# Optimization experiments

Measured on AMD Instinct MI355X. Metric: run time of the kernel, lower is better.

## Reference

```python
import jax, jax.numpy as jnp
import numpy as np

N = 100000        # nodes
E = 3200000       # edges (avg degree 32)
F_IN = 512        # input node features
HIDDEN = 16       # hardcoded in GCN.__init__
NUM_CLASSES = 40


def setup_inputs() -> dict:
    key = jax.random.key(0)
    k1, k2, k3, k4 = jax.random.split(key, 4)
    edge_index = jax.random.randint(k1, (2, E), 0, N, dtype=jnp.int32)
    x = jax.random.normal(k2, (N, F_IN), dtype=jnp.float32)
    # GCNConv weights (glorot-ish scale) and biases
    W1 = jax.random.normal(k3, (F_IN, HIDDEN), dtype=jnp.float32) * (1.0 / np.sqrt(F_IN))
    b1 = jnp.zeros((HIDDEN,), dtype=jnp.float32)
    W2 = jax.random.normal(k4, (HIDDEN, NUM_CLASSES), dtype=jnp.float32) * (1.0 / np.sqrt(HIDDEN))
    b2 = jnp.zeros((NUM_CLASSES,), dtype=jnp.float32)
    return {"edge_index": edge_index, "x": x, "W1": W1, "b1": b1, "W2": W2, "b2": b2}


def _gcn_conv(x, src, dst, W, b, n):
    # PyG GCNConv: linear transform, symmetric-normalized scatter-add aggregation
    h = x @ W                                             # [N, out]
    deg = jax.ops.segment_sum(jnp.ones_like(dst, dtype=h.dtype), dst, num_segments=n)
    dinv = jnp.where(deg > 0, jax.lax.rsqrt(deg), 0.0)    # deg^{-1/2}
    norm = dinv[src] * dinv[dst]                          # [E_total]
    out = jax.ops.segment_sum(h[src] * norm[:, None], dst, num_segments=n)
    return out + b


def reference(edge_index, x, W1, b1, W2, b2):
    n = x.shape[0]
    # GCNConv adds self-loops by default
    loop = jnp.arange(n, dtype=edge_index.dtype)
    src = jnp.concatenate([edge_index[0], loop])
    dst = jnp.concatenate([edge_index[1], loop])
    h = _gcn_conv(x, src, dst, W1, b1, n)
    h = jax.nn.relu(h)
    # F.dropout(training=self.training) -> identity in eval mode
    h = _gcn_conv(h, src, dst, W2, b2, n)
    return jax.nn.log_softmax(h, axis=1)[::20]
```

## Files before the change

### kernel.cpp

```cpp
#include <hip/hip_runtime.h>
#include <hip/hip_bf16.h>
#include <cstdint>
#include <math.h>

#define F_IN 512
#define HID  16
#define NCLS 40
#define OUT_STRIDE 20
#define TB   256
#define NBA  256
#define CAP  16384

typedef __attribute__((ext_vector_type(8))) short short8;
typedef __attribute__((ext_vector_type(4))) float f32x4;

__device__ inline unsigned short f2bf(float f) {
    unsigned u = __float_as_uint(f);
    u += 0x7fff + ((u >> 16) & 1);
    return (unsigned short)(u >> 16);
}
__device__ inline float bf2f(unsigned v) {
    return __uint_as_float(v << 16);
}

__global__ __launch_bounds__(256) void k_mega1(const float* __restrict__ x,
                                               const float* __restrict__ W1,
                                               unsigned short* __restrict__ h1b,
                                               const int* __restrict__ src,
                                               const int* __restrict__ dst,
                                               int* __restrict__ gcnt,
                                               unsigned* __restrict__ bin,
                                               int E, int NB, int chunk,
                                               int n, int GB) {
    __shared__ uint4 bl[16 * 64];
    int t = threadIdx.x;

    if ((int)blockIdx.x < GB) {
        for (int f = t; f < 16 * 64; f += 256) {
            int kstep = f >> 6, ln = f & 63;
            int col = ln & 15, k0 = kstep * 32 + (ln >> 4) * 8;
            unsigned up[4];
#pragma unroll
            for (int i = 0; i < 4; i++) {
                float a = W1[(k0 + 2 * i) * HID + col];
                float b = W1[(k0 + 2 * i + 1) * HID + col];
                up[i] = (unsigned)f2bf(a) | ((unsigned)f2bf(b) << 16);
            }
            bl[f] = make_uint4(up[0], up[1], up[2], up[3]);
        }
        __syncthreads();

        int wid = t >> 6, lane = t & 63;
        int rows0 = blockIdx.x * 256 + wid * 64;
        int arow = lane & 15, kgrp = lane >> 4;

        const float* xr[4];
#pragma unroll
        for (int rt = 0; rt < 4; rt++) {
            int r = rows0 + rt * 16 + arow;
            if (r >= n) r = n - 1;
            xr[rt] = x + (size_t)r * F_IN + kgrp * 8;
        }

        f32x4 acc[4];
#pragma unroll
        for (int rt = 0; rt < 4; rt++) acc[rt] = (f32x4){0.f, 0.f, 0.f, 0.f};

#pragma unroll 4
        for (int kstep = 0; kstep < 16; kstep++) {
            uint4 braw = bl[kstep * 64 + lane];
            short8 b;
            *(uint4*)&b = braw;
#pragma unroll
            for (int rt = 0; rt < 4; rt++) {
                f32x4 lo = __builtin_nontemporal_load((const f32x4*)(xr[rt] + kstep * 32));
                f32x4 hi = __builtin_nontemporal_load((const f32x4*)(xr[rt] + kstep * 32 + 4));
                __hip_bfloat162 c0 = __float22bfloat162_rn(make_float2(lo[0], lo[1]));
                __hip_bfloat162 c1 = __float22bfloat162_rn(make_float2(lo[2], lo[3]));
                __hip_bfloat162 c2 = __float22bfloat162_rn(make_float2(hi[0], hi[1]));
                __hip_bfloat162 c3 = __float22bfloat162_rn(make_float2(hi[2], hi[3]));
                uint4 araw;
                __builtin_memcpy(&araw.x, &c0, 4);
                __builtin_memcpy(&araw.y, &c1, 4);
                __builtin_memcpy(&araw.z, &c2, 4);
                __builtin_memcpy(&araw.w, &c3, 4);
                short8 a;
                *(uint4*)&a = araw;
                acc[rt] = __builtin_amdgcn_mfma_f32_16x16x32_bf16(a, b, acc[rt], 0, 0, 0);
            }
        }

        int col = lane & 15, rbase = (lane >> 4) * 4;
#pragma unroll
        for (int rt = 0; rt < 4; rt++) {
#pragma unroll
            for (int r = 0; r < 4; r++) {
                int row = rows0 + rt * 16 + rbase + r;
                if (row < n)
                    h1b[(size_t)row * HID + col] = f2bf(acc[rt][r]);
            }
        }
        return;
    }

    int blk = blockIdx.x - GB;
    int* h = (int*)bl;
    int* pos = h + 512;
    for (int b = t; b < NB; b += 256) h[b] = 0;
    __syncthreads();
    int e0 = blk * chunk, e1 = min(E, e0 + chunk);
    int nvec = (e1 - e0) >> 2;
    const int4* d4 = (const int4*)(dst + e0);
    const int4* s4 = (const int4*)(src + e0);
    for (int i = t; i < nvec; i += 256) {
        int4 d = d4[i];
        atomicAdd(&h[d.x >> 8], 1);
        atomicAdd(&h[d.y >> 8], 1);
        atomicAdd(&h[d.z >> 8], 1);
        atomicAdd(&h[d.w >> 8], 1);
    }
    for (int e = e0 + nvec * 4 + t; e < e1; e += 256)
        atomicAdd(&h[dst[e] >> 8], 1);
    __syncthreads();
    for (int b = t; b < NB; b += 256) {
        int c = h[b];
        int rb = c ? atomicAdd(&gcnt[b], c) : 0;
        pos[b] = b * CAP + rb;
    }
    __syncthreads();
    for (int i = t; i < nvec; i += 256) {
        int4 d = d4[i];
        int4 s = s4[i];
        int p;
        p = atomicAdd(&pos[d.x >> 8], 1); bin[p] = ((unsigned)s.x << 8) | (unsigned)(d.x & (TB - 1));
        p = atomicAdd(&pos[d.y >> 8], 1); bin[p] = ((unsigned)s.y << 8) | (unsigned)(d.y & (TB - 1));
        p = atomicAdd(&pos[d.z >> 8], 1); bin[p] = ((unsigned)s.z << 8) | (unsigned)(d.z & (TB - 1));
        p = atomicAdd(&pos[d.w >> 8], 1); bin[p] = ((unsigned)s.w << 8) | (unsigned)(d.w & (TB - 1));
    }
    for (int e = e0 + nvec * 4 + t; e < e1; e += 256) {
        int d = dst[e], s = src[e];
        int p = atomicAdd(&pos[d >> 8], 1);
        bin[p] = ((unsigned)s << 8) | (unsigned)(d & (TB - 1));
    }
}

__global__ __launch_bounds__(256) void k_sortb2(const unsigned* __restrict__ bin,
                                                const int* __restrict__ gcnt,
                                                int* __restrict__ csr,
                                                int2* __restrict__ rng,
                                                float* __restrict__ dinv,
                                                unsigned short* __restrict__ h1b,
                                                int N) {
    __shared__ int cnt[TB], incl[TB], pos[TB];
    int t = threadIdx.x, b = blockIdx.x;
    cnt[t] = 0;
    __syncthreads();
    int j0 = b * CAP, count = gcnt[b];
    for (int j = t; j < count; j += 256)
        atomicAdd(&cnt[bin[j0 + j] & (TB - 1)], 1);
    __syncthreads();
    incl[t] = cnt[t];
    __syncthreads();
    for (int off = 1; off < TB; off <<= 1) {
        int v = (t >= off) ? incl[t - off] : 0;
        __syncthreads();
        incl[t] += v;
        __syncthreads();
    }
    int ex = incl[t] - cnt[t];
    pos[t] = ex;
    int node = b * TB + t;
    float dv = rsqrtf((float)cnt[t] + 1.0f);
    if (node < N) {
        rng[node] = make_int2(j0 + ex, j0 + ex + cnt[t]);
        dinv[node] = dv;
        uint4* p = (uint4*)(h1b + (size_t)node * HID);
        uint4 lo = p[0], hi = p[1];
        unsigned w[8] = {lo.x, lo.y, lo.z, lo.w, hi.x, hi.y, hi.z, hi.w};
#pragma unroll
        for (int i = 0; i < 8; i++) {
            float a = bf2f(w[i] & 0xffff) * dv;
            float c = bf2f(w[i] >> 16) * dv;
            w[i] = (unsigned)f2bf(a) | ((unsigned)f2bf(c) << 16);
        }
        p[0] = make_uint4(w[0], w[1], w[2], w[3]);
        p[1] = make_uint4(w[4], w[5], w[6], w[7]);
    }
    __syncthreads();
    for (int j = t; j < count; j += 256) {
        unsigned v = bin[j0 + j];
        int pp = atomicAdd(&pos[v & (TB - 1)], 1);
        csr[j0 + pp] = (int)(v >> 8);
    }
}

__global__ __launch_bounds__(256) void k_agg(const uint2* __restrict__ h1u2,
                                             const int* __restrict__ csr,
                                             const int2* __restrict__ rng,
                                             const float* __restrict__ dinv,
                                             const float* __restrict__ b1,
                                             uint2* __restrict__ zu2, int n) {
    int lane = threadIdx.x & 63;
    int wave0 = (blockIdx.x * blockDim.x + threadIdx.x) >> 6;
    int nwaves = (gridDim.x * blockDim.x) >> 6;
    int c2 = lane & 3;
    int sub = lane >> 2;
    float bl0 = b1[4 * c2 + 0], bl1 = b1[4 * c2 + 1];
    float bl2 = b1[4 * c2 + 2], bl3 = b1[4 * c2 + 3];
    for (int node = wave0; node < n; node += nwaves) {
        int2 r = rng[node];
        int s0 = r.x, s1 = r.y;
        uint2 us = h1u2[(size_t)node * 4 + c2];
        float s[4] = {0.f, 0.f, 0.f, 0.f};
        int j = s0 + sub;
        int nxt = (j < s1) ? __builtin_nontemporal_load(&csr[j]) : 0;
        for (; j < s1; j += 16) {
            int cur = nxt;
            int jn = j + 16;
            if (jn < s1) nxt = __builtin_nontemporal_load(&csr[jn]);
            uint2 u = h1u2[(size_t)cur * 4 + c2];
            s[0] += bf2f(u.x & 0xffff); s[1] += bf2f(u.x >> 16);
            s[2] += bf2f(u.y & 0xffff); s[3] += bf2f(u.y >> 16);
        }
#pragma unroll
        for (int m = 4; m < 64; m <<= 1) {
            s[0] += __shfl_xor(s[0], m); s[1] += __shfl_xor(s[1], m);
            s[2] += __shfl_xor(s[2], m); s[3] += __shfl_xor(s[3], m);
        }
        s[0] += bf2f(us.x & 0xffff); s[1] += bf2f(us.x >> 16);
        s[2] += bf2f(us.y & 0xffff); s[3] += bf2f(us.y >> 16);
        float dv = dinv[node];
        float p0 = dv * s[0] + bl0;
        float p1 = dv * s[1] + bl1;
        float p2 = dv * s[2] + bl2;
        float p3 = dv * s[3] + bl3;
        if (lane < 4) {
            uint2 o;
            o.x = (unsigned)f2bf(fmaxf(p0, 0.f) * dv) | ((unsigned)f2bf(fmaxf(p1, 0.f) * dv) << 16);
            o.y = (unsigned)f2bf(fmaxf(p2, 0.f) * dv) | ((unsigned)f2bf(fmaxf(p3, 0.f) * dv) << 16);
            zu2[(size_t)node * 4 + c2] = o;
        }
    }
}

__global__ void k_out(const unsigned short* __restrict__ zb,
                      const int* __restrict__ csr, const int2* __restrict__ rng,
                      const float* __restrict__ dinv, const float* __restrict__ W2,
                      const float* __restrict__ b2, float* __restrict__ out, int nOut) {
    int lane = threadIdx.x & 63;
    int wv = (blockIdx.x * blockDim.x + threadIdx.x) >> 6;
    if (wv >= nOut) return;
    int node = wv * OUT_STRIDE;
    int c = lane & 15, sub = lane >> 4;
    int2 r = rng[node];
    int s0 = r.x, s1 = r.y;
    float sum = 0.f;
    for (int j = s0 + sub; j < s1; j += 4)
        sum += bf2f(zb[(size_t)__builtin_nontemporal_load(&csr[j]) * HID + c]);
    sum += __shfl_xor(sum, 16);
    sum += __shfl_xor(sum, 32);
    sum += bf2f(zb[(size_t)node * HID + c]);
    float a = dinv[node] * sum;

    int jj = lane < NCLS ? lane : 0;
    float v = 0.f;
#pragma unroll
    for (int cc = 0; cc < 16; cc++) {
        float ac = __shfl(a, cc);
        v = fmaf(ac, W2[cc * NCLS + jj], v);
    }
    v += b2[jj];

    float vm = lane < NCLS ? v : -INFINITY;
    for (int off = 1; off < 64; off <<= 1) vm = fmaxf(vm, __shfl_xor(vm, off));
    float ex = lane < NCLS ? expf(v - vm) : 0.f;
    float se = ex;
    for (int off = 1; off < 64; off <<= 1) se += __shfl_xor(se, off);
    float ls = logf(se);
    if (lane < NCLS) out[(size_t)wv * NCLS + lane] = v - vm - ls;
}

extern "C" void kernel_launch(void* const* d_in, const int* in_sizes, int n_in,
                              void* d_out, int out_size, void* d_ws, size_t ws_size,
                              hipStream_t stream) {
    const int E = in_sizes[0] / 2;
    const int N = in_sizes[1] / F_IN;
    const int nOut = (N + OUT_STRIDE - 1) / OUT_STRIDE;
    const int NB = (N + TB - 1) / TB;
    const int chunk = ((E + NBA - 1) / NBA + 3) & ~3;
    const int GB = (N + 255) / 256;

    const int* src = (const int*)d_in[0];
    const int* dst = src + E;
    const float* x  = (const float*)d_in[1];
    const float* W1 = (const float*)d_in[2];
    const float* b1 = (const float*)d_in[3];
    const float* W2 = (const float*)d_in[4];
    const float* b2 = (const float*)d_in[5];
    float* out = (float*)d_out;

    uint8_t* w = (uint8_t*)d_ws;
    size_t off = 0;
    auto carve = [&](size_t bytes) {
        void* p = w + off;
        off += (bytes + 15) & ~(size_t)15;
        return p;
    };
    float*          dinv  = (float*)carve((size_t)N * 4);
    int*            gcnt  = (int*)carve((size_t)NB * 4);
    unsigned*       bin   = (unsigned*)carve((size_t)NB * CAP * 4);
    int*            csr   = (int*)carve((size_t)NB * CAP * 4);
    int2*           rng   = (int2*)carve((size_t)N * 8);
    unsigned short* h1b   = (unsigned short*)carve((size_t)N * HID * 2);
    unsigned short* zb    = (unsigned short*)carve((size_t)N * HID * 2);
    (void)ws_size; (void)n_in; (void)out_size;

    (void)hipMemsetAsync(gcnt, 0, (size_t)NB * 4, stream);
    k_mega1<<<GB + NBA, 256, 0, stream>>>(x, W1, h1b, src, dst, gcnt, bin,
                                          E, NB, chunk, N, GB);
    k_sortb2<<<NB, TB, 0, stream>>>(bin, gcnt, csr, rng, dinv, h1b, N);
    k_agg  <<<2048, 256, 0, stream>>>((const uint2*)h1b, csr, rng, dinv, b1, (uint2*)zb, N);
    k_out  <<<(nOut * 64 + 255) / 256, 256, 0, stream>>>(zb, csr, rng, dinv, W2, b2, out, nOut);
}
```

Measured before the change: 171.9 us.

## Fuse all GCN stages into one cooperative persistent kernel with grid syncs

Replaces the four separate kernels with one cooperative kernel. Stage boundaries become grid.sync barriers, and the first 256 blocks do edge binning before joining a dynamic, atomic-counter tile queue for the x@W1 MFMA GEMM. This removes launch gaps between kernels and lets the binning and GEMM work balance across a persistent grid. In exchange, the grid is capped at 512-1024 blocks, so the later stages run with grid-stride loops instead of their original launch shapes, and each grid sync has its own cost.

```diff
diff --git a/kernel.cpp b/kernel.cpp
--- a/kernel.cpp
+++ b/kernel.cpp
@@ -1,14 +1,17 @@
 #include <hip/hip_runtime.h>
+#include <hip/hip_cooperative_groups.h>
 #include <hip/hip_bf16.h>
 #include <cstdint>
 #include <math.h>
+
+namespace cg = cooperative_groups;
 
 #define F_IN 512
 #define HID  16
 #define NCLS 40
 #define OUT_STRIDE 20
 #define TB   256
-#define NBA  256
+#define PARTB 256
 #define CAP  16384
 
 typedef __attribute__((ext_vector_type(8))) short short8;
@@ -23,261 +26,261 @@
     return __uint_as_float(v << 16);
 }
 
-__global__ __launch_bounds__(256) void k_mega1(const float* __restrict__ x,
-                                               const float* __restrict__ W1,
-                                               unsigned short* __restrict__ h1b,
-                                               const int* __restrict__ src,
-                                               const int* __restrict__ dst,
-                                               int* __restrict__ gcnt,
-                                               unsigned* __restrict__ bin,
-                                               int E, int NB, int chunk,
-                                               int n, int GB) {
+__global__ __launch_bounds__(256) void k_fused(
+    const float* __restrict__ x, const float* __restrict__ W1,
+    unsigned short* __restrict__ h1b,
+    const int* __restrict__ src, const int* __restrict__ dst,
+    int* __restrict__ gcnt, unsigned* __restrict__ bin,
+    int* __restrict__ csr, int2* __restrict__ rng, float* __restrict__ dinv,
+    unsigned short* __restrict__ zb, const float* __restrict__ b1,
+    const float* __restrict__ W2, const float* __restrict__ b2,
+    float* __restrict__ out,
+    int E, int N, int NB, int chunk, int GT, int* tilec, int nOut)
+{
+    cg::grid_group grid = cg::this_grid();
     __shared__ uint4 bl[16 * 64];
-    int t = threadIdx.x;
-
-    if ((int)blockIdx.x < GB) {
-        for (int f = t; f < 16 * 64; f += 256) {
-            int kstep = f >> 6, ln = f & 63;
-            int col = ln & 15, k0 = kstep * 32 + (ln >> 4) * 8;
-            unsigned up[4];
-#pragma unroll
-            for (int i = 0; i < 4; i++) {
-                float a = W1[(k0 + 2 * i) * HID + col];
-                float b = W1[(k0 + 2 * i + 1) * HID + col];
-                up[i] = (unsigned)f2bf(a) | ((unsigned)f2bf(b) << 16);
-            }
-            bl[f] = make_uint4(up[0], up[1], up[2], up[3]);
-        }
-        __syncthreads();
-
-        int wid = t >> 6, lane = t & 63;
-        int rows0 = blockIdx.x * 256 + wid * 64;
+    int t = threadIdx.x, blk = blockIdx.x;
+    int lane = t & 63;
+
+    if (blk < PARTB) {
+        int* h   = (int*)bl;
+        int* pos = h + 512;
+        for (int b = t; b < NB; b += 256) h[b] = 0;
+        __syncthreads();
+        int e0 = blk * chunk, e1 = min(E, e0 + chunk);
+        int nvec = (e1 - e0) >> 2;
+        const int4* d4 = (const int4*)(dst + e0);
+        const int4* s4 = (const int4*)(src + e0);
+        for (int i = t; i < nvec; i += 256) {
+            int4 d = d4[i];
+            atomicAdd(&h[d.x >> 8], 1);
+            atomicAdd(&h[d.y >> 8], 1);
+            atomicAdd(&h[d.z >> 8], 1);
+            atomicAdd(&h[d.w >> 8], 1);
+        }
+        for (int e = e0 + nvec * 4 + t; e < e1; e += 256)
+            atomicAdd(&h[dst[e] >> 8], 1);
+        __syncthreads();
+        for (int b = t; b < NB; b += 256) {
+            int c = h[b];
+            int rb = c ? atomicAdd(&gcnt[b], c) : 0;
+            pos[b] = b * CAP + rb;
+        }
+        __syncthreads();
+        for (int i = t; i < nvec; i += 256) {
+            int4 d = d4[i];
+            int4 s = s4[i];
+            int p;
+            p = atomicAdd(&pos[d.x >> 8], 1); bin[p] = ((unsigned)s.x << 8) | (unsigned)(d.x & (TB - 1));
+            p = atomicAdd(&pos[d.y >> 8], 1); bin[p] = ((unsigned)s.y << 8) | (unsigned)(d.y & (TB - 1));
+            p = atomicAdd(&pos[d.z >> 8], 1); bin[p] = ((unsigned)s.z << 8) | (unsigned)(d.z & (TB - 1));
+            p = atomicAdd(&pos[d.w >> 8], 1); bin[p] = ((unsigned)s.w << 8) | (unsigned)(d.w & (TB - 1));
+        }
+        for (int e = e0 + nvec * 4 + t; e < e1; e += 256) {
+            int d = dst[e], s = src[e];
+            int p = atomicAdd(&pos[d >> 8], 1);
+            bin[p] = ((unsigned)s << 8) | (unsigned)(d & (TB - 1));
+        }
+        __syncthreads();
+    }
+
+    for (int f = t; f < 16 * 64; f += 256) {
+        int kstep = f >> 6, ln = f & 63;
+        int col = ln & 15, k0 = kstep * 32 + (ln >> 4) * 8;
+        unsigned up[4];
+#pragma unroll
+        for (int i = 0; i < 4; i++) {
+            float a = W1[(k0 + 2 * i) * HID + col];
+            float b = W1[(k0 + 2 * i + 1) * HID + col];
+            up[i] = (unsigned)f2bf(a) | ((unsigned)f2bf(b) << 16);
+        }
+        bl[f] = make_uint4(up[0], up[1], up[2], up[3]);
+    }
+    __syncthreads();
+
+    {
         int arow = lane & 15, kgrp = lane >> 4;
-
-        const float* xr[4];
-#pragma unroll
-        for (int rt = 0; rt < 4; rt++) {
-            int r = rows0 + rt * 16 + arow;
-            if (r >= n) r = n - 1;
-            xr[rt] = x + (size_t)r * F_IN + kgrp * 8;
-        }
-
-        f32x4 acc[4];
-#pragma unroll
-        for (int rt = 0; rt < 4; rt++) acc[rt] = (f32x4){0.f, 0.f, 0.f, 0.f};
+        for (;;) {
+            int tl;
+            if (lane == 0) tl = atomicAdd(tilec, 1);
+            tl = __shfl(tl, 0);
+            if (tl >= GT) break;
+            int rows0 = tl * 64;
+
+            const float* xr[4];
+#pragma unroll
+            for (int rt = 0; rt < 4; rt++) {
+                int r = rows0 + rt * 16 + arow;
+                if (r >= N) r = N - 1;
+                xr[rt] = x + (size_t)r * F_IN + kgrp * 8;
+            }
+            f32x4 acc[4];
+#pragma unroll
+            for (int rt = 0; rt < 4; rt++) acc[rt] = (f32x4){0.f, 0.f, 0.f, 0.f};
 
 #pragma unroll 4
-        for (int kstep = 0; kstep < 16; kstep++) {
-            uint4 braw = bl[kstep * 64 + lane];
-            short8 b;
-            *(uint4*)&b = braw;
+            for (int kstep = 0; kstep < 16; kstep++) {
+                uint4 braw = bl[kstep * 64 + lane];
+                short8 b;
+                *(uint4*)&b = braw;
+#pragma unroll
+                for (int rt = 0; rt < 4; rt++) {
+                    f32x4 lo = __builtin_nontemporal_load((const f32x4*)(xr[rt] + kstep * 32));
+                    f32x4 hi = __builtin_nontemporal_load((const f32x4*)(xr[rt] + kstep * 32 + 4));
+                    __hip_bfloat162 c0 = __float22bfloat162_rn(make_float2(lo[0], lo[1]));
+                    __hip_bfloat162 c1 = __float22bfloat162_rn(make_float2(lo[2], lo[3]));
+                    __hip_bfloat162 c2 = __float22bfloat162_rn(make_float2(hi[0], hi[1]));
+                    __hip_bfloat162 c3 = __float22bfloat162_rn(make_float2(hi[2], hi[3]));
+                    uint4 araw;
+                    __builtin_memcpy(&araw.x, &c0, 4);
+                    __builtin_memcpy(&araw.y, &c1, 4);
+                    __builtin_memcpy(&araw.z, &c2, 4);
+                    __builtin_memcpy(&araw.w, &c3, 4);
+                    short8 a;
+                    *(uint4*)&a = araw;
+                    acc[rt] = __builtin_amdgcn_mfma_f32_16x16x32_bf16(a, b, acc[rt], 0, 0, 0);
+                }
+            }
+            int col = lane & 15, rbase = (lane >> 4) * 4;
 #pragma unroll
             for (int rt = 0; rt < 4; rt++) {
-                f32x4 lo = __builtin_nontemporal_load((const f32x4*)(xr[rt] + kstep * 32));
-                f32x4 hi = __builtin_nontemporal_load((const f32x4*)(xr[rt] + kstep * 32 + 4));
-                __hip_bfloat162 c0 = __float22bfloat162_rn(make_float2(lo[0], lo[1]));
-                __hip_bfloat162 c1 = __float22bfloat162_rn(make_float2(lo[2], lo[3]));
-                __hip_bfloat162 c2 = __float22bfloat162_rn(make_float2(hi[0], hi[1]));
-                __hip_bfloat162 c3 = __float22bfloat162_rn(make_float2(hi[2], hi[3]));
-                uint4 araw;
-                __builtin_memcpy(&araw.x, &c0, 4);
-                __builtin_memcpy(&araw.y, &c1, 4);
-                __builtin_memcpy(&araw.z, &c2, 4);
-                __builtin_memcpy(&araw.w, &c3, 4);
-                short8 a;
-                *(uint4*)&a = araw;
-                acc[rt] = __builtin_amdgcn_mfma_f32_16x16x32_bf16(a, b, acc[rt], 0, 0, 0);
-            }
-        }
-
-        int col = lane & 15, rbase = (lane >> 4) * 4;
-#pragma unroll
-        for (int rt = 0; rt < 4; rt++) {
-#pragma unroll
-            for (int r = 0; r < 4; r++) {
-                int row = rows0 + rt * 16 + rbase + r;
-                if (row < n)
-                    h1b[(size_t)row * HID + col] = f2bf(acc[rt][r]);
-            }
-        }
-        return;
-    }
-
-    int blk = blockIdx.x - GB;
-    int* h = (int*)bl;
-    int* pos = h + 512;
-    for (int b = t; b < NB; b += 256) h[b] = 0;
-    __syncthreads();
-    int e0 = blk * chunk, e1 = min(E, e0 + chunk);
-    int nvec = (e1 - e0) >> 2;
-    const int4* d4 = (const int4*)(dst + e0);
-    const int4* s4 = (const int4*)(src + e0);
-    for (int i = t; i < nvec; i += 256) {
-        int4 d = d4[i];
-        atomicAdd(&h[d.x >> 8], 1);
-        atomicAdd(&h[d.y >> 8], 1);
-        atomicAdd(&h[d.z >> 8], 1);
-        atomicAdd(&h[d.w >> 8], 1);
-    }
-    for (int e = e0 + nvec * 4 + t; e < e1; e += 256)
-        atomicAdd(&h[dst[e] >> 8], 1);
-    __syncthreads();
-    for (int b = t; b < NB; b += 256) {
-        int c = h[b];
-        int rb = c ? atomicAdd(&gcnt[b], c) : 0;
-        pos[b] = b * CAP + rb;
-    }
-    __syncthreads();
-    for (int i = t; i < nvec; i += 256) {
-        int4 d = d4[i];
-        int4 s = s4[i];
-        int p;
-        p = atomicAdd(&pos[d.x >> 8], 1); bin[p] = ((unsigned)s.x << 8) | (unsigned)(d.x & (TB - 1));
-        p = atomicAdd(&pos[d.y >> 8], 1); bin[p] = ((unsigned)s.y << 8) | (unsigned)(d.y & (TB - 1));
-        p = atomicAdd(&pos[d.z >> 8], 1); bin[p] = ((unsigned)s.z << 8) | (unsigned)(d.z & (TB - 1));
-        p = atomicAdd(&pos[d.w >> 8], 1); bin[p] = ((unsigned)s.w << 8) | (unsigned)(d.w & (TB - 1));
-    }
-    for (int e = e0 + nvec * 4 + t; e < e1; e += 256) {
-        int d = dst[e], s = src[e];
-        int p = atomicAdd(&pos[d >> 8], 1);
-        bin[p] = ((unsigned)s << 8) | (unsigned)(d & (TB - 1));
-    }
-}
-
-__global__ __launch_bounds__(256) void k_sortb2(const unsigned* __restrict__ bin,
-                                                const int* __restrict__ gcnt,
-                                                int* __restrict__ csr,
-                                                int2* __restrict__ rng,
-                                                float* __restrict__ dinv,
-                                                unsigned short* __restrict__ h1b,
-                                                int N) {
-    __shared__ int cnt[TB], incl[TB], pos[TB];
-    int t = threadIdx.x, b = blockIdx.x;
-    cnt[t] = 0;
-    __syncthreads();
-    int j0 = b * CAP, count = gcnt[b];
-    for (int j = t; j < count; j += 256)
-        atomicAdd(&cnt[bin[j0 + j] & (TB - 1)], 1);
-    __syncthreads();
-    incl[t] = cnt[t];
-    __syncthreads();
-    for (int off = 1; off < TB; off <<= 1) {
-        int v = (t >= off) ? incl[t - off] : 0;
-        __syncthreads();
-        incl[t] += v;
-        __syncthreads();
-    }
-    int ex = incl[t] - cnt[t];
-    pos[t] = ex;
-    int node = b * TB + t;
-    float dv = rsqrtf((float)cnt[t] + 1.0f);
-    if (node < N) {
-        rng[node] = make_int2(j0 + ex, j0 + ex + cnt[t]);
-        dinv[node] = dv;
-        uint4* p = (uint4*)(h1b + (size_t)node * HID);
-        uint4 lo = p[0], hi = p[1];
-        unsigned w[8] = {lo.x, lo.y, lo.z, lo.w, hi.x, hi.y, hi.z, hi.w};
-#pragma unroll
-        for (int i = 0; i < 8; i++) {
-            float a = bf2f(w[i] & 0xffff) * dv;
-            float c = bf2f(w[i] >> 16) * dv;
-            w[i] = (unsigned)f2bf(a) | ((unsigned)f2bf(c) << 16);
-        }
-        p[0] = make_uint4(w[0], w[1], w[2], w[3]);
-        p[1] = make_uint4(w[4], w[5], w[6], w[7]);
-    }
-    __syncthreads();
-    for (int j = t; j < count; j += 256) {
-        unsigned v = bin[j0 + j];
-        int pp = atomicAdd(&pos[v & (TB - 1)], 1);
-        csr[j0 + pp] = (int)(v >> 8);
-    }
-}
-
-__global__ __launch_bounds__(256) void k_agg(const uint2* __restrict__ h1u2,
-                                             const int* __restrict__ csr,
-                                             const int2* __restrict__ rng,
-                                             const float* __restrict__ dinv,
-                                             const float* __restrict__ b1,
-                                             uint2* __restrict__ zu2, int n) {
-    int lane = threadIdx.x & 63;
-    int wave0 = (blockIdx.x * blockDim.x + threadIdx.x) >> 6;
-    int nwaves = (gridDim.x * blockDim.x) >> 6;
-    int c2 = lane & 3;
-    int sub = lane >> 2;
-    float bl0 = b1[4 * c2 + 0], bl1 = b1[4 * c2 + 1];
-    float bl2 = b1[4 * c2 + 2], bl3 = b1[4 * c2 + 3];
-    for (int node = wave0; node < n; node += nwaves) {
-        int2 r = rng[node];
-        int s0 = r.x, s1 = r.y;
-        uint2 us = h1u2[(size_t)node * 4 + c2];
-        float s[4] = {0.f, 0.f, 0.f, 0.f};
-        int j = s0 + sub;
-        int nxt = (j < s1) ? __builtin_nontemporal_load(&csr[j]) : 0;
-        for (; j < s1; j += 16) {
-            int cur = nxt;
-            int jn = j + 16;
-            if (jn < s1) nxt = __builtin_nontemporal_load(&csr[jn]);
-            uint2 u = h1u2[(size_t)cur * 4 + c2];
-            s[0] += bf2f(u.x & 0xffff); s[1] += bf2f(u.x >> 16);
-            s[2] += bf2f(u.y & 0xffff); s[3] += bf2f(u.y >> 16);
-        }
-#pragma unroll
-        for (int m = 4; m < 64; m <<= 1) {
-            s[0] += __shfl_xor(s[0], m); s[1] += __shfl_xor(s[1], m);
-            s[2] += __shfl_xor(s[2], m); s[3] += __shfl_xor(s[3], m);
-        }
-        s[0] += bf2f(us.x & 0xffff); s[1] += bf2f(us.x >> 16);
-        s[2] += bf2f(us.y & 0xffff); s[3] += bf2f(us.y >> 16);
-        float dv = dinv[node];
-        float p0 = dv * s[0] + bl0;
-        float p1 = dv * s[1] + bl1;
-        float p2 = dv * s[2] + bl2;
-        float p3 = dv * s[3] + bl3;
-        if (lane < 4) {
-            uint2 o;
-            o.x = (unsigned)f2bf(fmaxf(p0, 0.f) * dv) | ((unsigned)f2bf(fmaxf(p1, 0.f) * dv) << 16);
-            o.y = (unsigned)f2bf(fmaxf(p2, 0.f) * dv) | ((unsigned)f2bf(fmaxf(p3, 0.f) * dv) << 16);
-            zu2[(size_t)node * 4 + c2] = o;
-        }
-    }
-}
-
-__global__ void k_out(const unsigned short* __restrict__ zb,
-                      const int* __restrict__ csr, const int2* __restrict__ rng,
-                      const float* __restrict__ dinv, const float* __restrict__ W2,
-                      const float* __restrict__ b2, float* __restrict__ out, int nOut) {
-    int lane = threadIdx.x & 63;
-    int wv = (blockIdx.x * blockDim.x + threadIdx.x) >> 6;
-    if (wv >= nOut) return;
-    int node = wv * OUT_STRIDE;
-    int c = lane & 15, sub = lane >> 4;
-    int2 r = rng[node];
-    int s0 = r.x, s1 = r.y;
-    float sum = 0.f;
-    for (int j = s0 + sub; j < s1; j += 4)
-        sum += bf2f(zb[(size_t)__builtin_nontemporal_load(&csr[j]) * HID + c]);
-    sum += __shfl_xor(sum, 16);
-    sum += __shfl_xor(sum, 32);
-    sum += bf2f(zb[(size_t)node * HID + c]);
-    float a = dinv[node] * sum;
-
-    int jj = lane < NCLS ? lane : 0;
-    float v = 0.f;
-#pragma unroll
-    for (int cc = 0; cc < 16; cc++) {
-        float ac = __shfl(a, cc);
-        v = fmaf(ac, W2[cc * NCLS + jj], v);
-    }
-    v += b2[jj];
-
-    float vm = lane < NCLS ? v : -INFINITY;
-    for (int off = 1; off < 64; off <<= 1) vm = fmaxf(vm, __shfl_xor(vm, off));
-    float ex = lane < NCLS ? expf(v - vm) : 0.f;
-    float se = ex;
-    for (int off = 1; off < 64; off <<= 1) se += __shfl_xor(se, off);
-    float ls = logf(se);
-    if (lane < NCLS) out[(size_t)wv * NCLS + lane] = v - vm - ls;
+#pragma unroll
+                for (int r = 0; r < 4; r++) {
+                    int row = rows0 + rt * 16 + rbase + r;
+                    if (row < N)
+                        h1b[(size_t)row * HID + col] = f2bf(acc[rt][r]);
+                }
+            }
+        }
+    }
+    grid.sync();
+
+    if (blk < NB) {
+        int* cnt  = (int*)bl;
+        int* incl = cnt + 256;
+        int* pos  = incl + 256;
+        cnt[t] = 0;
+        __syncthreads();
+        int j0 = blk * CAP, count = gcnt[blk];
+        for (int j = t; j < count; j += 256)
+            atomicAdd(&cnt[bin[j0 + j] & (TB - 1)], 1);
+        __syncthreads();
+        incl[t] = cnt[t];
+        __syncthreads();
+        for (int off = 1; off < TB; off <<= 1) {
+            int v = (t >= off) ? incl[t - off] : 0;
+            __syncthreads();
+            incl[t] += v;
+            __syncthreads();
+        }
+        int ex = incl[t] - cnt[t];
+        pos[t] = ex;
+        int node = blk * TB + t;
+        float dv = rsqrtf((float)cnt[t] + 1.0f);
+        if (node < N) {
+            rng[node] = make_int2(j0 + ex, j0 + ex + cnt[t]);
+            dinv[node] = dv;
+            uint4* p = (uint4*)(h1b + (size_t)node * HID);
+            uint4 lo = p[0], hi = p[1];
+            unsigned w[8] = {lo.x, lo.y, lo.z, lo.w, hi.x, hi.y, hi.z, hi.w};
+#pragma unroll
+            for (int i = 0; i < 8; i++) {
+                float a = bf2f(w[i] & 0xffff) * dv;
+                float c = bf2f(w[i] >> 16) * dv;
+                w[i] = (unsigned)f2bf(a) | ((unsigned)f2bf(c) << 16);
+            }
+            p[0] = make_uint4(w[0], w[1], w[2], w[3]);
+            p[1] = make_uint4(w[4], w[5], w[6], w[7]);
+        }
+        __syncthreads();
+        for (int j = t; j < count; j += 256) {
+            unsigned v = bin[j0 + j];
+            int pp = atomicAdd(&pos[v & (TB - 1)], 1);
+            csr[j0 + pp] = (int)(v >> 8);
+        }
+    }
+    grid.sync();
+
+    {
+        const uint2* h1u2 = (const uint2*)h1b;
+        uint2* zu2 = (uint2*)zb;
+        int wave0 = (blk * 256 + t) >> 6;
+        int nwaves = gridDim.x * 4;
+        int c2 = lane & 3;
+        int sub = lane >> 2;
+        float bl0 = b1[4 * c2 + 0], bl1 = b1[4 * c2 + 1];
+        float bl2 = b1[4 * c2 + 2], bl3 = b1[4 * c2 + 3];
+        for (int node = wave0; node < N; node += nwaves) {
+            int2 r = rng[node];
+            int s0 = r.x, s1 = r.y;
+            uint2 us = h1u2[(size_t)node * 4 + c2];
+            float s[4] = {0.f, 0.f, 0.f, 0.f};
+            int j = s0 + sub;
+            int nxt = (j < s1) ? __builtin_nontemporal_load(&csr[j]) : 0;
+            for (; j < s1; j += 16) {
+                int cur = nxt;
+                int jn = j + 16;
+                if (jn < s1) nxt = __builtin_nontemporal_load(&csr[jn]);
+                uint2 u = h1u2[(size_t)cur * 4 + c2];
+                s[0] += bf2f(u.x & 0xffff); s[1] += bf2f(u.x >> 16);
+                s[2] += bf2f(u.y & 0xffff); s[3] += bf2f(u.y >> 16);
+            }
+#pragma unroll
+            for (int m = 4; m < 64; m <<= 1) {
+                s[0] += __shfl_xor(s[0], m); s[1] += __shfl_xor(s[1], m);
+                s[2] += __shfl_xor(s[2], m); s[3] += __shfl_xor(s[3], m);
+            }
+            s[0] += bf2f(us.x & 0xffff); s[1] += bf2f(us.x >> 16);
+            s[2] += bf2f(us.y & 0xffff); s[3] += bf2f(us.y >> 16);
+            float dv = dinv[node];
+            float p0 = dv * s[0] + bl0;
+            float p1 = dv * s[1] + bl1;
+            float p2 = dv * s[2] + bl2;
+            float p3 = dv * s[3] + bl3;
+            if (lane < 4) {
+                uint2 o;
+                o.x = (unsigned)f2bf(fmaxf(p0, 0.f) * dv) | ((unsigned)f2bf(fmaxf(p1, 0.f) * dv) << 16);
+                o.y = (unsigned)f2bf(fmaxf(p2, 0.f) * dv) | ((unsigned)f2bf(fmaxf(p3, 0.f) * dv) << 16);
+                zu2[(size_t)node * 4 + c2] = o;
+            }
+        }
+    }
+    grid.sync();
+
+    {
+        int wave0 = (blk * 256 + t) >> 6;
+        int nwaves = gridDim.x * 4;
+        int c = lane & 15, sub = lane >> 4;
+        for (int wv = wave0; wv < nOut; wv += nwaves) {
+            int node = wv * OUT_STRIDE;
+            int2 r = rng[node];
+            int s0 = r.x, s1 = r.y;
+            float sum = 0.f;
+            for (int j = s0 + sub; j < s1; j += 4)
+                sum += bf2f(zb[(size_t)__builtin_nontemporal_load(&csr[j]) * HID + c]);
+            sum += __shfl_xor(sum, 16);
+            sum += __shfl_xor(sum, 32);
+            sum += bf2f(zb[(size_t)node * HID + c]);
+            float a = dinv[node] * sum;
+
+            int jj = lane < NCLS ? lane : 0;
+            float v = 0.f;
+#pragma unroll
+            for (int cc = 0; cc < 16; cc++) {
+                float ac = __shfl(a, cc);
+                v = fmaf(ac, W2[cc * NCLS + jj], v);
+            }
+            v += b2[jj];
+
+            float vm = lane < NCLS ? v : -INFINITY;
+            for (int off = 1; off < 64; off <<= 1) vm = fmaxf(vm, __shfl_xor(vm, off));
+            float ex = lane < NCLS ? expf(v - vm) : 0.f;
+            float se = ex;
+            for (int off = 1; off < 64; off <<= 1) se += __shfl_xor(se, off);
+            float ls = logf(se);
+            if (lane < NCLS) out[(size_t)wv * NCLS + lane] = v - vm - ls;
+        }
+    }
 }
 
 extern "C" void kernel_launch(void* const* d_in, const int* in_sizes, int n_in,
@@ -287,16 +290,16 @@
     const int N = in_sizes[1] / F_IN;
     const int nOut = (N + OUT_STRIDE - 1) / OUT_STRIDE;
     const int NB = (N + TB - 1) / TB;
-    const int chunk = ((E + NBA - 1) / NBA + 3) & ~3;
-    const int GB = (N + 255) / 256;
-
-    const int* src = (const int*)d_in[0];
-    const int* dst = src + E;
+    const int chunk = ((E + PARTB - 1) / PARTB + 3) & ~3;
+    const int GT = (N + 63) / 64;
+
     const float* x  = (const float*)d_in[1];
     const float* W1 = (const float*)d_in[2];
     const float* b1 = (const float*)d_in[3];
     const float* W2 = (const float*)d_in[4];
     const float* b2 = (const float*)d_in[5];
+    const int* src = (const int*)d_in[0];
+    const int* dst = src + E;
     float* out = (float*)d_out;
 
     uint8_t* w = (uint8_t*)d_ws;
@@ -307,18 +310,30 @@
         return p;
     };
     float*          dinv  = (float*)carve((size_t)N * 4);
-    int*            gcnt  = (int*)carve((size_t)NB * 4);
+    int*            gcnt  = (int*)carve((size_t)(NB + 4) * 4);
     unsigned*       bin   = (unsigned*)carve((size_t)NB * CAP * 4);
     int*            csr   = (int*)carve((size_t)NB * CAP * 4);
     int2*           rng   = (int2*)carve((size_t)N * 8);
     unsigned short* h1b   = (unsigned short*)carve((size_t)N * HID * 2);
     unsigned short* zb    = (unsigned short*)carve((size_t)N * HID * 2);
+    int*            tilec = gcnt + NB;
     (void)ws_size; (void)n_in; (void)out_size;
 
-    (void)hipMemsetAsync(gcnt, 0, (size_t)NB * 4, stream);
-    k_mega1<<<GB + NBA, 256, 0, stream>>>(x, W1, h1b, src, dst, gcnt, bin,
-                                          E, NB, chunk, N, GB);
-    k_sortb2<<<NB, TB, 0, stream>>>(bin, gcnt, csr, rng, dinv, h1b, N);
-    k_agg  <<<2048, 256, 0, stream>>>((const uint2*)h1b, csr, rng, dinv, b1, (uint2*)zb, N);
-    k_out  <<<(nOut * 64 + 255) / 256, 256, 0, stream>>>(zb, csr, rng, dinv, W2, b2, out, nOut);
+    int maxb = 0;
+    if (hipOccupancyMaxActiveBlocksPerMultiprocessor(&maxb, k_fused, 256, 0)
+        != hipSuccess || maxb < 2) maxb = 2;
+    int grid = maxb * 256;
+    if (grid > 1024) grid = 1024;
+    if (grid < 512)  grid = 512;
+
+    (void)hipMemsetAsync(gcnt, 0, (size_t)(NB + 4) * 4, stream);
+
+    int Ee = E, Nn = N, NBv = NB, chv = chunk, GTv = GT, nOv = nOut;
+    void* ka[] = {(void*)&x, (void*)&W1, (void*)&h1b, (void*)&src, (void*)&dst,
+                  (void*)&gcnt, (void*)&bin, (void*)&csr, (void*)&rng, (void*)&dinv,
+                  (void*)&zb, (void*)&b1, (void*)&W2, (void*)&b2, (void*)&out,
+                  (void*)&Ee, (void*)&Nn, (void*)&NBv, (void*)&chv, (void*)&GTv,
+                  (void*)&tilec, (void*)&nOv};
+    (void)hipLaunchCooperativeKernel((void*)k_fused, dim3(grid), dim3(256),
+                                     ka, 0, stream);
 }
```

Measured after the change: 467.6 us. +172.0%, slower.

## Use atomic work-stealing of GEMM tiles across all blocks in fused first kernel

Applied to the files above, without the earlier changes.

The fused first kernel no longer splits blocks statically into GEMM blocks and edge-partition blocks. Every block, including the edge-binning blocks once they finish partitioning, now pulls 64-row GEMM tiles from a global atomic counter, one per wavefront, until all tiles are done. This aims to balance load between the memory-bound x@W1 projection and the atomic-heavy binning so neither phase leaves CUs idle. It adds a global atomic per tile and hardcodes the GEMM block count to 391.

```diff
diff --git a/kernel.cpp b/kernel.cpp
--- a/kernel.cpp
+++ b/kernel.cpp
@@ -8,7 +8,7 @@
 #define NCLS 40
 #define OUT_STRIDE 20
 #define TB   256
-#define NBA  256
+#define PARTB 256
 #define CAP  16384
 
 typedef __attribute__((ext_vector_type(8))) short short8;
@@ -30,29 +30,77 @@
                                                const int* __restrict__ dst,
                                                int* __restrict__ gcnt,
                                                unsigned* __restrict__ bin,
+                                               int* __restrict__ tilec,
                                                int E, int NB, int chunk,
-                                               int n, int GB) {
+                                               int n, int GT, int GB) {
     __shared__ uint4 bl[16 * 64];
     int t = threadIdx.x;
-
-    if ((int)blockIdx.x < GB) {
-        for (int f = t; f < 16 * 64; f += 256) {
-            int kstep = f >> 6, ln = f & 63;
-            int col = ln & 15, k0 = kstep * 32 + (ln >> 4) * 8;
-            unsigned up[4];
-#pragma unroll
-            for (int i = 0; i < 4; i++) {
-                float a = W1[(k0 + 2 * i) * HID + col];
-                float b = W1[(k0 + 2 * i + 1) * HID + col];
-                up[i] = (unsigned)f2bf(a) | ((unsigned)f2bf(b) << 16);
-            }
-            bl[f] = make_uint4(up[0], up[1], up[2], up[3]);
-        }
-        __syncthreads();
-
-        int wid = t >> 6, lane = t & 63;
-        int rows0 = blockIdx.x * 256 + wid * 64;
-        int arow = lane & 15, kgrp = lane >> 4;
+    int lane = t & 63;
+
+    if ((int)blockIdx.x >= GB) {
+        int blk = blockIdx.x - GB;
+        int* h = (int*)bl;
+        int* pos = h + 512;
+        for (int b = t; b < NB; b += 256) h[b] = 0;
+        __syncthreads();
+        int e0 = blk * chunk, e1 = min(E, e0 + chunk);
+        int nvec = (e1 - e0) >> 2;
+        const int4* d4 = (const int4*)(dst + e0);
+        const int4* s4 = (const int4*)(src + e0);
+        for (int i = t; i < nvec; i += 256) {
+            int4 d = d4[i];
+            atomicAdd(&h[d.x >> 8], 1);
+            atomicAdd(&h[d.y >> 8], 1);
+            atomicAdd(&h[d.z >> 8], 1);
+            atomicAdd(&h[d.w >> 8], 1);
+        }
+        for (int e = e0 + nvec * 4 + t; e < e1; e += 256)
+            atomicAdd(&h[dst[e] >> 8], 1);
+        __syncthreads();
+        for (int b = t; b < NB; b += 256) {
+            int c = h[b];
+            int rb = c ? atomicAdd(&gcnt[b], c) : 0;
+            pos[b] = b * CAP + rb;
+        }
+        __syncthreads();
+        for (int i = t; i < nvec; i += 256) {
+            int4 d = d4[i];
+            int4 s = s4[i];
+            int p;
+            p = atomicAdd(&pos[d.x >> 8], 1); bin[p] = ((unsigned)s.x << 8) | (unsigned)(d.x & (TB - 1));
+            p = atomicAdd(&pos[d.y >> 8], 1); bin[p] = ((unsigned)s.y << 8) | (unsigned)(d.y & (TB - 1));
+            p = atomicAdd(&pos[d.z >> 8], 1); bin[p] = ((unsigned)s.z << 8) | (unsigned)(d.z & (TB - 1));
+            p = atomicAdd(&pos[d.w >> 8], 1); bin[p] = ((unsigned)s.w << 8) | (unsigned)(d.w & (TB - 1));
+        }
+        for (int e = e0 + nvec * 4 + t; e < e1; e += 256) {
+            int d = dst[e], s = src[e];
+            int p = atomicAdd(&pos[d >> 8], 1);
+            bin[p] = ((unsigned)s << 8) | (unsigned)(d & (TB - 1));
+        }
+        __syncthreads();
+    }
+
+    for (int f = t; f < 16 * 64; f += 256) {
+        int kstep = f >> 6, ln = f & 63;
+        int col = ln & 15, k0 = kstep * 32 + (ln >> 4) * 8;
+        unsigned up[4];
+#pragma unroll
+        for (int i = 0; i < 4; i++) {
+            float a = W1[(k0 + 2 * i) * HID + col];
+            float b = W1[(k0 + 2 * i + 1) * HID + col];
+            up[i] = (unsigned)f2bf(a) | ((unsigned)f2bf(b) << 16);
+        }
+        bl[f] = make_uint4(up[0], up[1], up[2], up[3]);
+    }
+    __syncthreads();
+
+    int arow = lane & 15, kgrp = lane >> 4;
+    for (;;) {
+        int tl;
+        if (lane == 0) tl = atomicAdd(tilec, 1);
+        tl = __shfl(tl, 0);
+        if (tl >= GT) break;
+        int rows0 = tl * 64;
 
         const float* xr[4];
 #pragma unroll
@@ -61,7 +109,6 @@
             if (r >= n) r = n - 1;
             xr[rt] = x + (size_t)r * F_IN + kgrp * 8;
         }
-
         f32x4 acc[4];
 #pragma unroll
         for (int rt = 0; rt < 4; rt++) acc[rt] = (f32x4){0.f, 0.f, 0.f, 0.f};
@@ -89,7 +136,6 @@
                 acc[rt] = __builtin_amdgcn_mfma_f32_16x16x32_bf16(a, b, acc[rt], 0, 0, 0);
             }
         }
-
         int col = lane & 15, rbase = (lane >> 4) * 4;
 #pragma unroll
         for (int rt = 0; rt < 4; rt++) {
@@ -100,47 +146,6 @@
                     h1b[(size_t)row * HID + col] = f2bf(acc[rt][r]);
             }
         }
-        return;
-    }
-
-    int blk = blockIdx.x - GB;
-    int* h = (int*)bl;
-    int* pos = h + 512;
-    for (int b = t; b < NB; b += 256) h[b] = 0;
-    __syncthreads();
-    int e0 = blk * chunk, e1 = min(E, e0 + chunk);
-    int nvec = (e1 - e0) >> 2;
-    const int4* d4 = (const int4*)(dst + e0);
-    const int4* s4 = (const int4*)(src + e0);
-    for (int i = t; i < nvec; i += 256) {
-        int4 d = d4[i];
-        atomicAdd(&h[d.x >> 8], 1);
-        atomicAdd(&h[d.y >> 8], 1);
-        atomicAdd(&h[d.z >> 8], 1);
-        atomicAdd(&h[d.w >> 8], 1);
-    }
-    for (int e = e0 + nvec * 4 + t; e < e1; e += 256)
-        atomicAdd(&h[dst[e] >> 8], 1);
-    __syncthreads();
-    for (int b = t; b < NB; b += 256) {
-        int c = h[b];
-        int rb = c ? atomicAdd(&gcnt[b], c) : 0;
-        pos[b] = b * CAP + rb;
-    }
-    __syncthreads();
-    for (int i = t; i < nvec; i += 256) {
-        int4 d = d4[i];
-        int4 s = s4[i];
-        int p;
-        p = atomicAdd(&pos[d.x >> 8], 1); bin[p] = ((unsigned)s.x << 8) | (unsigned)(d.x & (TB - 1));
-        p = atomicAdd(&pos[d.y >> 8], 1); bin[p] = ((unsigned)s.y << 8) | (unsigned)(d.y & (TB - 1));
-        p = atomicAdd(&pos[d.z >> 8], 1); bin[p] = ((unsigned)s.z << 8) | (unsigned)(d.z & (TB - 1));
-        p = atomicAdd(&pos[d.w >> 8], 1); bin[p] = ((unsigned)s.w << 8) | (unsigned)(d.w & (TB - 1));
-    }
-    for (int e = e0 + nvec * 4 + t; e < e1; e += 256) {
-        int d = dst[e], s = src[e];
-        int p = atomicAdd(&pos[d >> 8], 1);
-        bin[p] = ((unsigned)s << 8) | (unsigned)(d & (TB - 1));
     }
 }
 
@@ -287,8 +292,9 @@
     const int N = in_sizes[1] / F_IN;
     const int nOut = (N + OUT_STRIDE - 1) / OUT_STRIDE;
     const int NB = (N + TB - 1) / TB;
-    const int chunk = ((E + NBA - 1) / NBA + 3) & ~3;
-    const int GB = (N + 255) / 256;
+    const int chunk = ((E + PARTB - 1) / PARTB + 3) & ~3;
+    const int GT = (N + 63) / 64;
+    const int GB = 391;
 
     const int* src = (const int*)d_in[0];
     const int* dst = src + E;
@@ -307,17 +313,18 @@
         return p;
     };
     float*          dinv  = (float*)carve((size_t)N * 4);
-    int*            gcnt  = (int*)carve((size_t)NB * 4);
+    int*            gcnt  = (int*)carve((size_t)(NB + 4) * 4);
     unsigned*       bin   = (unsigned*)carve((size_t)NB * CAP * 4);
     int*            csr   = (int*)carve((size_t)NB * CAP * 4);
     int2*           rng   = (int2*)carve((size_t)N * 8);
     unsigned short* h1b   = (unsigned short*)carve((size_t)N * HID * 2);
     unsigned short* zb    = (unsigned short*)carve((size_t)N * HID * 2);
+    int*            tilec = gcnt + NB;
     (void)ws_size; (void)n_in; (void)out_size;
 
-    (void)hipMemsetAsync(gcnt, 0, (size_t)NB * 4, stream);
-    k_mega1<<<GB + NBA, 256, 0, stream>>>(x, W1, h1b, src, dst, gcnt, bin,
-                                          E, NB, chunk, N, GB);
+    (void)hipMemsetAsync(gcnt, 0, (size_t)(NB + 4) * 4, stream);
+    k_mega1<<<GB + PARTB, 256, 0, stream>>>(x, W1, h1b, src, dst, gcnt, bin,
+                                            tilec, E, NB, chunk, N, GT, GB);
     k_sortb2<<<NB, TB, 0, stream>>>(bin, gcnt, csr, rng, dinv, h1b, N);
     k_agg  <<<2048, 256, 0, stream>>>((const uint2*)h1b, csr, rng, dinv, b1, (uint2*)zb, N);
     k_out  <<<(nOut * 64 + 255) / 256, 256, 0, stream>>>(zb, csr, rng, dinv, W2, b2, out, nOut);
```

Result: slower. 192.3 us (+11.9%).
